# Optimization experiments

Measured on AMD Instinct MI355X. Metric: run time of the kernel, lower is better.

The kernel has to match this reference:

```python
import jax, jax.numpy as jnp
import numpy as np
from jax import lax

# Dimensions (ModelArgs with d_model=1024)
B, L = 2, 1024
D_MODEL = 1024
D_INNER = 2048          # expand * d_model
D_STATE = 16
DT_RANK = 64            # ceil(d_model / 16)
D_CONV = 4


def setup_inputs() -> dict:
    key = jax.random.key(0)
    ks = jax.random.split(key, 8)
    sc = lambda k, shp, s: jax.random.normal(k, shp, dtype=jnp.float32) * s
    x = jax.random.normal(ks[0], (B, L, D_MODEL), dtype=jnp.float32)
    W_in = sc(ks[1], (2 * D_INNER, D_MODEL), 0.02)
    conv_w = sc(ks[2], (D_INNER, D_CONV), 0.2)
    conv_b = jnp.zeros((D_INNER,), jnp.float32)
    W_x = sc(ks[3], (DT_RANK + 2 * D_STATE, D_INNER), 0.02)
    dt_init_std = DT_RANK ** -0.5
    W_dt = jax.random.uniform(ks[4], (D_INNER, DT_RANK), jnp.float32,
                              -dt_init_std, dt_init_std)
    # dt_proj bias: inverse-softplus of dt ~ logUniform(dt_min, dt_max)
    dt_min, dt_max = 1e-3, 1e-1
    u = jax.random.uniform(ks[5], (D_INNER,), jnp.float32)
    dt = jnp.exp(u * (np.log(dt_max) - np.log(dt_min)) + np.log(dt_min))
    dt = jnp.clip(dt, 1e-4, None)
    b_dt = dt + jnp.log(-jnp.expm1(-dt))
    A_log = jnp.log(jnp.tile(jnp.arange(1, D_STATE + 1, dtype=jnp.float32)[None, :],
                             (D_INNER, 1)))
    D = jnp.ones((D_INNER,), jnp.float32)
    W_out = sc(ks[6], (D_MODEL, D_INNER), 0.02)
    return {"x": x, "W_in": W_in, "conv_w": conv_w, "conv_b": conv_b,
            "W_x": W_x, "W_dt": W_dt, "b_dt": b_dt, "A_log": A_log,
            "D": D, "W_out": W_out}


def reference(x, W_in, conv_w, conv_b, W_x, W_dt, b_dt, A_log, D, W_out):
    b, l, _ = x.shape
    d_in, n = A_log.shape
    k = conv_w.shape[1]

    # in_proj, split into conv branch and gating residual
    x_and_res = x @ W_in.T                                 # (b, l, 2*d_in)
    xz, res = jnp.split(x_and_res, [d_in], axis=-1)

    # Causal depthwise conv1d (kernel k, left-pad k-1, truncate to l)
    xp = jnp.pad(xz, ((0, 0), (k - 1, 0), (0, 0)))         # (b, l+k-1, d_in)
    xc = conv_b[None, None, :] + sum(
        xp[:, i:i + l, :] * conv_w[None, None, :, i] for i in range(k))
    xc = jax.nn.silu(xc)                                   # (b, l, d_in)

    # x_proj -> delta, B, C
    x_dbl = xc @ W_x.T                                     # (b, l, dt_rank+2n)
    dlt, Bm, Cm = jnp.split(x_dbl, [DT_RANK, DT_RANK + n], axis=-1)
    delta = jax.nn.softplus(dlt @ W_dt.T + b_dt)           # (b, l, d_in)

    # selective scan
    A = -jnp.exp(A_log)                                    # (d_in, n)
    dA = jnp.exp(delta[..., None] * A[None, None])         # (b, l, d_in, n)
    dBu = (delta * xc)[..., None] * Bm[:, :, None, :]      # (b, l, d_in, n)

    def step(h, inp):
        dA_t, dBu_t, C_t = inp                             # (b,d,n),(b,d,n),(b,n)
        h = dA_t * h + dBu_t
        y = jnp.einsum('bdn,bn->bd', h, C_t)
        return h, y

    h0 = jnp.zeros((b, d_in, n), xc.dtype)
    _, ys = lax.scan(step, h0, (dA.transpose(1, 0, 2, 3),
                                dBu.transpose(1, 0, 2, 3),
                                Cm.transpose(1, 0, 2)))
    y = ys.transpose(1, 0, 2) + xc * D[None, None, :]      # (b, l, d_in)

    y = y * jax.nn.silu(res)
    return y @ W_out.T                                     # (b, l, d_model)
```

## Files before the change

kernel.cpp:

```cpp
#include <hip/hip_runtime.h>
#include <hip/hip_bf16.h>
#include <cmath>

#define DEV __device__ __forceinline__

typedef float  f32x4  __attribute__((ext_vector_type(4)));
typedef __bf16 bf16x8 __attribute__((ext_vector_type(8)));
using u16 = unsigned short;

constexpr int CB   = 2;
constexpr int CLEN = 1024;
constexpr int CDM  = 1024;
constexpr int CDI  = 2048;
constexpr int CM   = CB * CLEN;
constexpr int NCHUNK = 64;
constexpr int CHL    = 16;

DEV u16 f2bf(float f) {
  unsigned u = __builtin_bit_cast(unsigned, f);
  unsigned r = (u + 0x7fffu + ((u >> 16) & 1u)) >> 16;
  return (u16)r;
}
DEV float bf2f(u16 v) { return __builtin_bit_cast(float, ((unsigned)v) << 16); }

DEV ushort4 f4bf(float4 v) {
  ushort4 o;
  o.x = f2bf(v.x); o.y = f2bf(v.y); o.z = f2bf(v.z); o.w = f2bf(v.w);
  return o;
}

constexpr int CG_X   = 524288;
constexpr int CG_WIN = CG_X   + 1048576;
constexpr int CG_WDT = CG_WIN + 32768;
constexpr int CG_WO  = CG_WDT + 524288;
constexpr int CG_WX  = CG_WO  + 65536;

__global__ void cast_all_k(const float* __restrict__ x, const float* __restrict__ W_in,
                           const float* __restrict__ W_dt, const float* __restrict__ W_out,
                           const float* __restrict__ W_x,
                           u16* __restrict__ xb, u16* __restrict__ W_inb,
                           u16* __restrict__ W_dtb, u16* __restrict__ W_outb,
                           u16* __restrict__ W_xb)
{
  int i = blockIdx.x * blockDim.x + threadIdx.x;
  if (i < CG_X) {
    reinterpret_cast<ushort4*>(xb)[i] = f4bf(reinterpret_cast<const float4*>(x)[i]);
  } else if (i < CG_WIN) {
    int j = i - CG_X;
    reinterpret_cast<ushort4*>(W_inb)[j] = f4bf(reinterpret_cast<const float4*>(W_in)[j]);
  } else if (i < CG_WDT) {
    int j = i - CG_WIN;
    reinterpret_cast<ushort4*>(W_dtb)[j] = f4bf(reinterpret_cast<const float4*>(W_dt)[j]);
  } else if (i < CG_WO) {
    int j = i - CG_WDT;
    reinterpret_cast<ushort4*>(W_outb)[j] = f4bf(reinterpret_cast<const float4*>(W_out)[j]);
  } else {
    int j = i - CG_WO;
    int base = j * 4, row = base >> 11, col = base & 2047;
    float4 v = make_float4(0.f, 0.f, 0.f, 0.f);
    if (row < 96) v = *reinterpret_cast<const float4*>(W_x + row * 2048 + col);
    reinterpret_cast<ushort4*>(W_xb)[j] = f4bf(v);
  }
}

DEV void gload_lds16(const void* g, void* l) {
  __builtin_amdgcn_global_load_lds(
      (const __attribute__((address_space(1))) void*)g,
      (__attribute__((address_space(3))) void*)l, 16, 0, 0);
}

template <int EPI, int SPLITK>
__global__ __launch_bounds__(256, 2)
void gemm_bt(const u16* __restrict__ A, const u16* __restrict__ Bw,
             float* __restrict__ C, u16* __restrict__ Cb,
             const float* __restrict__ bias,
             int Nd, int Kd, int lda, int ldb, int ldc, size_t slice_stride)
{
  __shared__ u16 As[128 * 32];
  __shared__ u16 Bs[128 * 32];
  const int tid  = threadIdx.x;
  const int wave = tid >> 6;
  const int lane = tid & 63;
  const int wm = wave >> 1, wn = wave & 1;
  const int row0 = blockIdx.y * 128;
  const int col0 = blockIdx.x * 128;
  const int lr = lane >> 2;
  const int lc = (lane & 3) * 8;

  const int kper = Kd / SPLITK;
  const int kbeg = (SPLITK > 1) ? blockIdx.z * kper : 0;
  float* Cz = (SPLITK > 1) ? C + (size_t)blockIdx.z * slice_stride : C;

  f32x4 acc[4][4] = {};

  for (int k0 = kbeg; k0 < kbeg + kper; k0 += 32) {
#pragma unroll
    for (int j = 0; j < 2; ++j) {
      const int rb = j * 64 + wave * 16;
      gload_lds16(A  + (size_t)(row0 + rb + lr) * lda + k0 + lc, As + rb * 32);
      gload_lds16(Bw + (size_t)(col0 + rb + lr) * ldb + k0 + lc, Bs + rb * 32);
    }
    __syncthreads();

    const int q  = lane >> 4;
    const int mr = lane & 15;
    bf16x8 af[4], bfr[4];
#pragma unroll
    for (int t = 0; t < 4; ++t) {
      af[t]  = *reinterpret_cast<const bf16x8*>(As + (wm * 64 + t * 16 + mr) * 32 + q * 8);
      bfr[t] = *reinterpret_cast<const bf16x8*>(Bs + (wn * 64 + t * 16 + mr) * 32 + q * 8);
    }
#pragma unroll
    for (int mt = 0; mt < 4; ++mt)
#pragma unroll
      for (int nt = 0; nt < 4; ++nt)
        acc[mt][nt] = __builtin_amdgcn_mfma_f32_16x16x32_bf16(af[mt], bfr[nt], acc[mt][nt], 0, 0, 0);
    __syncthreads();
  }

  const int q  = lane >> 4;
  const int cn = lane & 15;
#pragma unroll
  for (int mt = 0; mt < 4; ++mt)
#pragma unroll
    for (int nt = 0; nt < 4; ++nt)
#pragma unroll
      for (int r = 0; r < 4; ++r) {
        const int row = row0 + wm * 64 + mt * 16 + q * 4 + r;
        const int col = col0 + wn * 64 + nt * 16 + cn;
        float v = acc[mt][nt][r];
        if (EPI == 3) {
          v += bias[col];
          v = (v > 15.f) ? v : log1pf(__expf(v));
        }
        if (EPI == 0) Cz[(size_t)row * ldc + col] = v;
        else          Cb[(size_t)row * ldc + col] = f2bf(v);
      }
}

__global__ void xdbl_reduce_k(const float* __restrict__ part,
                              float* __restrict__ xdbl, u16* __restrict__ xdblb)
{
  int i = blockIdx.x * blockDim.x + threadIdx.x;
  float4 s = reinterpret_cast<const float4*>(part)[i];
#pragma unroll
  for (int z = 1; z < 8; ++z) {
    float4 p = reinterpret_cast<const float4*>(part + (size_t)z * CM * 128)[i];
    s.x += p.x; s.y += p.y; s.z += p.z; s.w += p.w;
  }
  reinterpret_cast<float4*>(xdbl)[i] = s;
  reinterpret_cast<ushort4*>(xdblb)[i] = f4bf(s);
}

__global__ void out_reduce_k(const float* __restrict__ part, float* __restrict__ out)
{
  int i = blockIdx.x * blockDim.x + threadIdx.x;
  float4 s = reinterpret_cast<const float4*>(part)[i];
#pragma unroll
  for (int z = 1; z < 4; ++z) {
    float4 p = reinterpret_cast<const float4*>(part + (size_t)z * CM * CDM)[i];
    s.x += p.x; s.y += p.y; s.z += p.z; s.w += p.w;
  }
  reinterpret_cast<float4*>(out)[i] = s;
}

__global__ void conv_silu_k(const u16* __restrict__ xzb, const float4* __restrict__ cw4,
                            const float* __restrict__ cb,
                            u16* __restrict__ xcb, u16* __restrict__ rsb)
{
  int idx = blockIdx.x * blockDim.x + threadIdx.x;
  int d   = idx & (CDI - 1);
  int row = idx >> 11;
  int l   = row & (CLEN - 1);
  float4 wv = cw4[d];
  const float* wp = (const float*)&wv;
  float acc = cb[d];
#pragma unroll
  for (int i = 0; i < 4; ++i) {
    int ls = l - 3 + i;
    float v = (ls >= 0) ? bf2f(xzb[(size_t)(row - l + ls) * 4096 + d]) : 0.f;
    acc += v * wp[i];
  }
  float s = acc / (1.f + __expf(-acc));
  xcb[idx] = f2bf(s);
  float r = bf2f(xzb[(size_t)row * 4096 + CDI + d]);
  rsb[idx] = f2bf(r / (1.f + __expf(-r)));
}

__global__ __launch_bounds__(256)
void scan_p1(const u16* __restrict__ delta_b, const u16* __restrict__ xcb,
             const float* __restrict__ xdbl, const float* __restrict__ A_log,
             float* __restrict__ P, float* __restrict__ S)
{
  __shared__ float sB[CHL * 16];
  const int t = threadIdx.x;
  const int d = blockIdx.x * 256 + t;
  const int c = blockIdx.y, b = blockIdx.z;

  if (t < CHL * 16) {
    int ll = t >> 4, n = t & 15;
    sB[t] = xdbl[(size_t)(b * CLEN + c * CHL + ll) * 128 + 64 + n];
  }
  __syncthreads();

  float An[16], Pv[16], Sv[16];
#pragma unroll
  for (int n = 0; n < 16; ++n) {
    An[n] = -__expf(A_log[d * 16 + n]);
    Pv[n] = 1.f; Sv[n] = 0.f;
  }
  const size_t rbase = (size_t)(b * CLEN + c * CHL) * CDI + d;
  for (int ll = 0; ll < CHL; ++ll) {
    float dl = bf2f(delta_b[rbase + (size_t)ll * CDI]);
    float u  = bf2f(xcb[rbase + (size_t)ll * CDI]);
    float du = dl * u;
#pragma unroll
    for (int n = 0; n < 16; ++n) {
      float a = __expf(dl * An[n]);
      Pv[n] *= a;
      Sv[n] = a * Sv[n] + du * sB[ll * 16 + n];
    }
  }
  const size_t o = (size_t)((b * NCHUNK + c) * 16) * CDI + d;
#pragma unroll
  for (int n = 0; n < 16; ++n) {
    P[o + (size_t)n * CDI] = Pv[n];
    S[o + (size_t)n * CDI] = Sv[n];
  }
}

__global__ void scan_p2(const float* __restrict__ P, const float* __restrict__ S,
                        float* __restrict__ Hin)
{
  const int t = threadIdx.x;
  const int d = blockIdx.x * 256 + t;
  const int n = blockIdx.y, b = blockIdx.z;
  float h = 0.f;
#pragma unroll 8
  for (int c = 0; c < NCHUNK; ++c) {
    size_t o = (size_t)((b * NCHUNK + c) * 16 + n) * CDI + d;
    Hin[o] = h;
    h = P[o] * h + S[o];
  }
}

__global__ __launch_bounds__(256)
void scan_p3(const u16* __restrict__ delta_b, const u16* __restrict__ xcb,
             const float* __restrict__ xdbl, const float* __restrict__ A_log,
             const float* __restrict__ Dvec, const u16* __restrict__ rsb,
             const float* __restrict__ Hin, u16* __restrict__ ybarb)
{
  __shared__ float sB[CHL * 16];
  __shared__ float sC[CHL * 16];
  const int t = threadIdx.x;
  const int d = blockIdx.x * 256 + t;
  const int c = blockIdx.y, b = blockIdx.z;

  if (t < CHL * 16) {
    int ll = t >> 4, n = t & 15;
    size_t ro = (size_t)(b * CLEN + c * CHL + ll) * 128;
    sB[t] = xdbl[ro + 64 + n];
    sC[t] = xdbl[ro + 80 + n];
  }
  __syncthreads();

  float An[16], h[16];
  const size_t ho = (size_t)((b * NCHUNK + c) * 16) * CDI + d;
#pragma unroll
  for (int n = 0; n < 16; ++n) {
    An[n] = -__expf(A_log[d * 16 + n]);
    h[n]  = Hin[ho + (size_t)n * CDI];
  }
  const float Dd = Dvec[d];
  const size_t rbase = (size_t)(b * CLEN + c * CHL);
  for (int ll = 0; ll < CHL; ++ll) {
    size_t e = (rbase + ll) * CDI + d;
    float dl = bf2f(delta_b[e]);
    float u  = bf2f(xcb[e]);
    float du = dl * u;
    float y  = 0.f;
#pragma unroll
    for (int n = 0; n < 16; ++n) {
      float a = __expf(dl * An[n]);
      h[n] = a * h[n] + du * sB[ll * 16 + n];
      y += h[n] * sC[ll * 16 + n];
    }
    y += u * Dd;
    ybarb[e] = f2bf(y * bf2f(rsb[e]));
  }
}

extern "C" void kernel_launch(void* const* d_in, const int* in_sizes, int n_in,
                              void* d_out, int out_size, void* d_ws, size_t ws_size,
                              hipStream_t stream)
{
  (void)in_sizes; (void)n_in; (void)out_size; (void)ws_size;
  const float* x      = (const float*)d_in[0];
  const float* W_in   = (const float*)d_in[1];
  const float* conv_w = (const float*)d_in[2];
  const float* conv_b = (const float*)d_in[3];
  const float* W_x    = (const float*)d_in[4];
  const float* W_dt   = (const float*)d_in[5];
  const float* b_dt   = (const float*)d_in[6];
  const float* A_log  = (const float*)d_in[7];
  const float* Dvec   = (const float*)d_in[8];
  const float* W_out  = (const float*)d_in[9];
  float* out = (float*)d_out;

  constexpr size_t MB = 1048576;
  char* w = (char*)d_ws;
  u16*   xzres_b = (u16*)(w + 0);
  u16*   xb      = (u16*)(w + 16 * MB);
  u16*   W_inb   = (u16*)(w + 20 * MB);
  float* xpart   = (float*)(w + 28 * MB);
  float* opart   = (float*)(w + 0);
  float* Pb      = (float*)(w + 36 * MB);
  float* Sb      = (float*)(w + 52 * MB);
  float* Hin     = (float*)(w + 68 * MB);
  u16*   xcb     = (u16*)(w + 84 * MB);
  u16*   rsb     = (u16*)(w + 92 * MB);
  float* xdbl    = (float*)(w + 100 * MB);
  u16*   xdblb   = (u16*)(w + 101 * MB);
  u16*   W_xb    = (u16*)(w + 101 * MB + 512 * 1024);
  u16*   W_dtb   = (u16*)(w + 102 * MB);
  u16*   delta_b = (u16*)(w + 102 * MB + 256 * 1024);
  u16*   ybarb   = (u16*)(w + 110 * MB + 256 * 1024);
  u16*   W_outb  = (u16*)(w + 118 * MB + 256 * 1024);

  dim3 blk(256);
  cast_all_k<<<CG_WX / 256, blk, 0, stream>>>(x, W_in, W_dt, W_out, W_x,
                                              xb, W_inb, W_dtb, W_outb, W_xb);
  gemm_bt<1, 1><<<dim3(32, 16), blk, 0, stream>>>(xb, W_inb, nullptr, xzres_b, nullptr,
                                                  4096, 1024, 1024, 1024, 4096, 0);
  conv_silu_k<<<(CB * CLEN * CDI) / 256, blk, 0, stream>>>(xzres_b, (const float4*)conv_w,
                                                           conv_b, xcb, rsb);
  gemm_bt<0, 8><<<dim3(1, 16, 8), blk, 0, stream>>>(xcb, W_xb, xpart, nullptr, nullptr,
                                                    128, 2048, 2048, 2048, 128,
                                                    (size_t)CM * 128);
  xdbl_reduce_k<<<(CM * 128 / 4) / 256, blk, 0, stream>>>(xpart, xdbl, xdblb);
  gemm_bt<3, 1><<<dim3(16, 16), blk, 0, stream>>>(xdblb, W_dtb, nullptr, delta_b, b_dt,
                                                  2048, 64, 128, 64, 2048, 0);
  scan_p1<<<dim3(8, NCHUNK, 2), blk, 0, stream>>>(delta_b, xcb, xdbl, A_log, Pb, Sb);
  scan_p2<<<dim3(8, 16, 2), blk, 0, stream>>>(Pb, Sb, Hin);
  scan_p3<<<dim3(8, NCHUNK, 2), blk, 0, stream>>>(delta_b, xcb, xdbl, A_log, Dvec, rsb,
                                                  Hin, ybarb);
  gemm_bt<0, 4><<<dim3(8, 16, 4), blk, 0, stream>>>(ybarb, W_outb, opart, nullptr, nullptr,
                                                    1024, 2048, 2048, 2048, 1024,
                                                    (size_t)CM * CDM);
  out_reduce_k<<<(CM * CDM / 4) / 256, blk, 0, stream>>>(opart, out);
}
```

Before: 254.1 us.

## Replace split-K reduce kernels with atomics and interleave delta/xc for scan

Split-K GEMMs for x_proj and out_proj now accumulate with float atomics into buffers zeroed by the cast kernel, removing the separate partial-sum reduction kernels and their partial buffers. Delta and the conv output are stored interleaved so the scan kernels read one 32-bit word per element. The silu of the residual is computed inside scan_p3 instead of in a separate stored tensor. Scan chunk length rises from 16 to 32. Atomics make the summation order nondeterministic and can add contention.

```diff
diff --git a/kernel.cpp b/kernel.cpp
--- a/kernel.cpp
+++ b/kernel.cpp
@@ -7,14 +7,15 @@
 typedef float  f32x4  __attribute__((ext_vector_type(4)));
 typedef __bf16 bf16x8 __attribute__((ext_vector_type(8)));
 using u16 = unsigned short;
+using u32 = unsigned int;
 
 constexpr int CB   = 2;
 constexpr int CLEN = 1024;
 constexpr int CDM  = 1024;
 constexpr int CDI  = 2048;
 constexpr int CM   = CB * CLEN;
-constexpr int NCHUNK = 64;
-constexpr int CHL    = 16;
+constexpr int NCHUNK = 32;
+constexpr int CHL    = 32;
 
 DEV u16 f2bf(float f) {
   unsigned u = __builtin_bit_cast(unsigned, f);
@@ -34,13 +35,16 @@
 constexpr int CG_WDT = CG_WIN + 32768;
 constexpr int CG_WO  = CG_WDT + 524288;
 constexpr int CG_WX  = CG_WO  + 65536;
+constexpr int CG_ZO  = CG_WX  + 524288;
+constexpr int CG_ZX  = CG_ZO  + 65536;
 
 __global__ void cast_all_k(const float* __restrict__ x, const float* __restrict__ W_in,
                            const float* __restrict__ W_dt, const float* __restrict__ W_out,
                            const float* __restrict__ W_x,
                            u16* __restrict__ xb, u16* __restrict__ W_inb,
                            u16* __restrict__ W_dtb, u16* __restrict__ W_outb,
-                           u16* __restrict__ W_xb)
+                           u16* __restrict__ W_xb,
+                           float* __restrict__ out_z, float* __restrict__ xdbl_z)
 {
   int i = blockIdx.x * blockDim.x + threadIdx.x;
   if (i < CG_X) {
@@ -54,12 +58,16 @@
   } else if (i < CG_WO) {
     int j = i - CG_WDT;
     reinterpret_cast<ushort4*>(W_outb)[j] = f4bf(reinterpret_cast<const float4*>(W_out)[j]);
-  } else {
+  } else if (i < CG_WX) {
     int j = i - CG_WO;
     int base = j * 4, row = base >> 11, col = base & 2047;
     float4 v = make_float4(0.f, 0.f, 0.f, 0.f);
     if (row < 96) v = *reinterpret_cast<const float4*>(W_x + row * 2048 + col);
     reinterpret_cast<ushort4*>(W_xb)[j] = f4bf(v);
+  } else if (i < CG_ZO) {
+    reinterpret_cast<float4*>(out_z)[i - CG_WX] = make_float4(0.f, 0.f, 0.f, 0.f);
+  } else {
+    reinterpret_cast<float4*>(xdbl_z)[i - CG_ZO] = make_float4(0.f, 0.f, 0.f, 0.f);
   }
 }
 
@@ -74,7 +82,7 @@
 void gemm_bt(const u16* __restrict__ A, const u16* __restrict__ Bw,
              float* __restrict__ C, u16* __restrict__ Cb,
              const float* __restrict__ bias,
-             int Nd, int Kd, int lda, int ldb, int ldc, size_t slice_stride)
+             int Nd, int Kd, int lda, int ldb, int ldc)
 {
   __shared__ u16 As[128 * 32];
   __shared__ u16 Bs[128 * 32];
@@ -89,7 +97,6 @@
 
   const int kper = Kd / SPLITK;
   const int kbeg = (SPLITK > 1) ? blockIdx.z * kper : 0;
-  float* Cz = (SPLITK > 1) ? C + (size_t)blockIdx.z * slice_stride : C;
 
   f32x4 acc[4][4] = {};
 
@@ -129,44 +136,31 @@
         const int row = row0 + wm * 64 + mt * 16 + q * 4 + r;
         const int col = col0 + wn * 64 + nt * 16 + cn;
         float v = acc[mt][nt][r];
-        if (EPI == 3) {
+        if (EPI == 0) {
+          C[(size_t)row * ldc + col] = v;
+        } else if (EPI == 1) {
+          Cb[(size_t)row * ldc + col] = f2bf(v);
+        } else if (EPI == 3) {
           v += bias[col];
           v = (v > 15.f) ? v : log1pf(__expf(v));
+          Cb[((size_t)row * ldc + col) * 2] = f2bf(v);
+        } else {
+          unsafeAtomicAdd(&C[(size_t)row * ldc + col], v);
         }
-        if (EPI == 0) Cz[(size_t)row * ldc + col] = v;
-        else          Cb[(size_t)row * ldc + col] = f2bf(v);
       }
 }
 
-__global__ void xdbl_reduce_k(const float* __restrict__ part,
-                              float* __restrict__ xdbl, u16* __restrict__ xdblb)
+__global__ void xdbl_cast_k(const float* __restrict__ xdbl, u16* __restrict__ xdblb)
 {
   int i = blockIdx.x * blockDim.x + threadIdx.x;
-  float4 s = reinterpret_cast<const float4*>(part)[i];
-#pragma unroll
-  for (int z = 1; z < 8; ++z) {
-    float4 p = reinterpret_cast<const float4*>(part + (size_t)z * CM * 128)[i];
-    s.x += p.x; s.y += p.y; s.z += p.z; s.w += p.w;
-  }
-  reinterpret_cast<float4*>(xdbl)[i] = s;
-  reinterpret_cast<ushort4*>(xdblb)[i] = f4bf(s);
-}
-
-__global__ void out_reduce_k(const float* __restrict__ part, float* __restrict__ out)
-{
-  int i = blockIdx.x * blockDim.x + threadIdx.x;
-  float4 s = reinterpret_cast<const float4*>(part)[i];
-#pragma unroll
-  for (int z = 1; z < 4; ++z) {
-    float4 p = reinterpret_cast<const float4*>(part + (size_t)z * CM * CDM)[i];
-    s.x += p.x; s.y += p.y; s.z += p.z; s.w += p.w;
-  }
-  reinterpret_cast<float4*>(out)[i] = s;
+  int base = i * 4, row = base >> 6, col = base & 63;
+  float4 v = *reinterpret_cast<const float4*>(xdbl + row * 128 + col);
+  reinterpret_cast<ushort4*>(xdblb)[i] = f4bf(v);
 }
 
 __global__ void conv_silu_k(const u16* __restrict__ xzb, const float4* __restrict__ cw4,
                             const float* __restrict__ cb,
-                            u16* __restrict__ xcb, u16* __restrict__ rsb)
+                            u16* __restrict__ xcb, u16* __restrict__ dxc)
 {
   int idx = blockIdx.x * blockDim.x + threadIdx.x;
   int d   = idx & (CDI - 1);
@@ -182,14 +176,14 @@
     acc += v * wp[i];
   }
   float s = acc / (1.f + __expf(-acc));
-  xcb[idx] = f2bf(s);
-  float r = bf2f(xzb[(size_t)row * 4096 + CDI + d]);
-  rsb[idx] = f2bf(r / (1.f + __expf(-r)));
+  u16 sb = f2bf(s);
+  xcb[idx] = sb;
+  dxc[2 * (size_t)idx + 1] = sb;
 }
 
 __global__ __launch_bounds__(256)
-void scan_p1(const u16* __restrict__ delta_b, const u16* __restrict__ xcb,
-             const float* __restrict__ xdbl, const float* __restrict__ A_log,
+void scan_p1(const u32* __restrict__ dxc, const float* __restrict__ xdbl,
+             const float* __restrict__ A_log,
              float* __restrict__ P, float* __restrict__ S)
 {
   __shared__ float sB[CHL * 16];
@@ -197,9 +191,9 @@
   const int d = blockIdx.x * 256 + t;
   const int c = blockIdx.y, b = blockIdx.z;
 
-  if (t < CHL * 16) {
-    int ll = t >> 4, n = t & 15;
-    sB[t] = xdbl[(size_t)(b * CLEN + c * CHL + ll) * 128 + 64 + n];
+  for (int i = t; i < CHL * 16; i += 256) {
+    int ll = i >> 4, n = i & 15;
+    sB[i] = xdbl[(size_t)(b * CLEN + c * CHL + ll) * 128 + 64 + n];
   }
   __syncthreads();
 
@@ -211,8 +205,9 @@
   }
   const size_t rbase = (size_t)(b * CLEN + c * CHL) * CDI + d;
   for (int ll = 0; ll < CHL; ++ll) {
-    float dl = bf2f(delta_b[rbase + (size_t)ll * CDI]);
-    float u  = bf2f(xcb[rbase + (size_t)ll * CDI]);
+    u32 pv = dxc[rbase + (size_t)ll * CDI];
+    float dl = bf2f((u16)(pv & 0xffffu));
+    float u  = bf2f((u16)(pv >> 16));
     float du = dl * u;
 #pragma unroll
     for (int n = 0; n < 16; ++n) {
@@ -245,10 +240,10 @@
 }
 
 __global__ __launch_bounds__(256)
-void scan_p3(const u16* __restrict__ delta_b, const u16* __restrict__ xcb,
-             const float* __restrict__ xdbl, const float* __restrict__ A_log,
-             const float* __restrict__ Dvec, const u16* __restrict__ rsb,
-             const float* __restrict__ Hin, u16* __restrict__ ybarb)
+void scan_p3(const u32* __restrict__ dxc, const float* __restrict__ xdbl,
+             const float* __restrict__ A_log, const float* __restrict__ Dvec,
+             const u16* __restrict__ xzb, const float* __restrict__ Hin,
+             u16* __restrict__ ybarb)
 {
   __shared__ float sB[CHL * 16];
   __shared__ float sC[CHL * 16];
@@ -256,11 +251,11 @@
   const int d = blockIdx.x * 256 + t;
   const int c = blockIdx.y, b = blockIdx.z;
 
-  if (t < CHL * 16) {
-    int ll = t >> 4, n = t & 15;
+  for (int i = t; i < CHL * 16; i += 256) {
+    int ll = i >> 4, n = i & 15;
     size_t ro = (size_t)(b * CLEN + c * CHL + ll) * 128;
-    sB[t] = xdbl[ro + 64 + n];
-    sC[t] = xdbl[ro + 80 + n];
+    sB[i] = xdbl[ro + 64 + n];
+    sC[i] = xdbl[ro + 80 + n];
   }
   __syncthreads();
 
@@ -275,8 +270,9 @@
   const size_t rbase = (size_t)(b * CLEN + c * CHL);
   for (int ll = 0; ll < CHL; ++ll) {
     size_t e = (rbase + ll) * CDI + d;
-    float dl = bf2f(delta_b[e]);
-    float u  = bf2f(xcb[e]);
+    u32 pv = dxc[e];
+    float dl = bf2f((u16)(pv & 0xffffu));
+    float u  = bf2f((u16)(pv >> 16));
     float du = dl * u;
     float y  = 0.f;
 #pragma unroll
@@ -286,7 +282,9 @@
       y += h[n] * sC[ll * 16 + n];
     }
     y += u * Dd;
-    ybarb[e] = f2bf(y * bf2f(rsb[e]));
+    float r = bf2f(xzb[(rbase + ll) * 4096 + CDI + d]);
+    float sr = r / (1.f + __expf(-r));
+    ybarb[e] = f2bf(y * sr);
   }
 }
 
@@ -312,40 +310,35 @@
   u16*   xzres_b = (u16*)(w + 0);
   u16*   xb      = (u16*)(w + 16 * MB);
   u16*   W_inb   = (u16*)(w + 20 * MB);
-  float* xpart   = (float*)(w + 28 * MB);
-  float* opart   = (float*)(w + 0);
-  float* Pb      = (float*)(w + 36 * MB);
-  float* Sb      = (float*)(w + 52 * MB);
-  float* Hin     = (float*)(w + 68 * MB);
-  u16*   xcb     = (u16*)(w + 84 * MB);
-  u16*   rsb     = (u16*)(w + 92 * MB);
-  float* xdbl    = (float*)(w + 100 * MB);
-  u16*   xdblb   = (u16*)(w + 101 * MB);
-  u16*   W_xb    = (u16*)(w + 101 * MB + 512 * 1024);
-  u16*   W_dtb   = (u16*)(w + 102 * MB);
-  u16*   delta_b = (u16*)(w + 102 * MB + 256 * 1024);
-  u16*   ybarb   = (u16*)(w + 110 * MB + 256 * 1024);
-  u16*   W_outb  = (u16*)(w + 118 * MB + 256 * 1024);
+  u16*   xcb     = (u16*)(w + 28 * MB);
+  u16*   dxc     = (u16*)(w + 36 * MB);
+  float* xdbl    = (float*)(w + 52 * MB);
+  u16*   xdblb   = (u16*)(w + 53 * MB);
+  u16*   W_xb    = (u16*)(w + 53 * MB + 256 * 1024);
+  u16*   W_dtb   = (u16*)(w + 53 * MB + 768 * 1024);
+  float* Pb      = (float*)(w + 54 * MB);
+  float* Sb      = (float*)(w + 62 * MB);
+  float* Hin     = (float*)(w + 70 * MB);
+  u16*   ybarb   = (u16*)(w + 78 * MB);
+  u16*   W_outb  = (u16*)(w + 86 * MB);
 
   dim3 blk(256);
-  cast_all_k<<<CG_WX / 256, blk, 0, stream>>>(x, W_in, W_dt, W_out, W_x,
-                                              xb, W_inb, W_dtb, W_outb, W_xb);
+  cast_all_k<<<CG_ZX / 256, blk, 0, stream>>>(x, W_in, W_dt, W_out, W_x,
+                                              xb, W_inb, W_dtb, W_outb, W_xb,
+                                              out, xdbl);
   gemm_bt<1, 1><<<dim3(32, 16), blk, 0, stream>>>(xb, W_inb, nullptr, xzres_b, nullptr,
-                                                  4096, 1024, 1024, 1024, 4096, 0);
+                                                  4096, 1024, 1024, 1024, 4096);
   conv_silu_k<<<(CB * CLEN * CDI) / 256, blk, 0, stream>>>(xzres_b, (const float4*)conv_w,
-                                                           conv_b, xcb, rsb);
-  gemm_bt<0, 8><<<dim3(1, 16, 8), blk, 0, stream>>>(xcb, W_xb, xpart, nullptr, nullptr,
-                                                    128, 2048, 2048, 2048, 128,
-                                                    (size_t)CM * 128);
-  xdbl_reduce_k<<<(CM * 128 / 4) / 256, blk, 0, stream>>>(xpart, xdbl, xdblb);
-  gemm_bt<3, 1><<<dim3(16, 16), blk, 0, stream>>>(xdblb, W_dtb, nullptr, delta_b, b_dt,
-                                                  2048, 64, 128, 64, 2048, 0);
-  scan_p1<<<dim3(8, NCHUNK, 2), blk, 0, stream>>>(delta_b, xcb, xdbl, A_log, Pb, Sb);
+                                                           conv_b, xcb, dxc);
+  gemm_bt<4, 16><<<dim3(1, 16, 16), blk, 0, stream>>>(xcb, W_xb, xdbl, nullptr, nullptr,
+                                                      128, 2048, 2048, 2048, 128);
+  xdbl_cast_k<<<(CM * 64 / 4) / 256, blk, 0, stream>>>(xdbl, xdblb);
+  gemm_bt<3, 1><<<dim3(16, 16), blk, 0, stream>>>(xdblb, W_dtb, nullptr, dxc, b_dt,
+                                                  2048, 64, 64, 64, 2048);
+  scan_p1<<<dim3(8, NCHUNK, 2), blk, 0, stream>>>((const u32*)dxc, xdbl, A_log, Pb, Sb);
   scan_p2<<<dim3(8, 16, 2), blk, 0, stream>>>(Pb, Sb, Hin);
-  scan_p3<<<dim3(8, NCHUNK, 2), blk, 0, stream>>>(delta_b, xcb, xdbl, A_log, Dvec, rsb,
-                                                  Hin, ybarb);
-  gemm_bt<0, 4><<<dim3(8, 16, 4), blk, 0, stream>>>(ybarb, W_outb, opart, nullptr, nullptr,
-                                                    1024, 2048, 2048, 2048, 1024,
-                                                    (size_t)CM * CDM);
-  out_reduce_k<<<(CM * CDM / 4) / 256, blk, 0, stream>>>(opart, out);
-}
+  scan_p3<<<dim3(8, NCHUNK, 2), blk, 0, stream>>>((const u32*)dxc, xdbl, A_log, Dvec,
+                                                  xzres_b, Hin, ybarb);
+  gemm_bt<4, 4><<<dim3(8, 16, 4), blk, 0, stream>>>(ybarb, W_outb, out, nullptr, nullptr,
+                                                    1024, 2048, 2048, 2048, 1024);
+}
```

New measurement: 280.1 us. 10.2% more time.
